# Kernel tuning notes

Measured on AMD Instinct MI355X. Metric: run time of the kernel, lower is better.

Reference implementation:

```python
import jax, jax.numpy as jnp
import numpy as np

B, P, J, MOT, K, NB, WN, H = 64, 12273, 80, 94, 64, 20, 17, 128
W_POSE = 1.0

def euler_to_rotmat(a):
    # a: [..., 3] radians, R = Rz @ Ry @ Rx
    sx, sy, sz = jnp.sin(a[..., 0]), jnp.sin(a[..., 1]), jnp.sin(a[..., 2])
    cx, cy, cz = jnp.cos(a[..., 0]), jnp.cos(a[..., 1]), jnp.cos(a[..., 2])
    r00 = cz * cy; r01 = cz * sy * sx - sz * cx; r02 = cz * sy * cx + sz * sx
    r10 = sz * cy; r11 = sz * sy * sx + cz * cx; r12 = sz * sy * cx - cz * sx
    r20 = -sy;     r21 = cy * sx;                r22 = cy * cx
    return jnp.stack([jnp.stack([r00, r01, r02], -1),
                      jnp.stack([r10, r11, r12], -1),
                      jnp.stack([r20, r21, r22], -1)], -2)

def setup_inputs() -> dict:
    key = jax.random.key(0)
    ks = jax.random.split(key, 20)
    f32 = jnp.float32
    return {
        'in_pc_batch': jax.random.normal(ks[0], (B, P, 3), f32),
        't_nor': jax.random.normal(ks[1], (B, P, 3), f32),
        'rest_verts': jax.random.normal(ks[2], (P, 3), f32),
        'skin_weights': jax.random.uniform(ks[3], (P, J), f32),
        'mul_weight_list': jax.random.normal(ks[4], (J, MOT), f32),
        'query': jax.random.normal(ks[5], (B, J, 3), f32),
        'cloth_pose_std': jax.random.uniform(ks[6], (3,), f32),
        'cloth_pose_mean': jax.random.normal(ks[7], (3,), f32),
        'cloth_trans_std': jax.random.uniform(ks[8], (3,), f32),
        'cloth_trans_mean': jax.random.normal(ks[9], (3,), f32),
        'W1': jax.random.normal(ks[10], (3 + K, H), f32) * 0.1,
        'b1': jnp.zeros((H,), f32),
        'W2': jax.random.normal(ks[11], (H, 6), f32) * 0.1,
        'b2': jnp.zeros((6,), f32),
        'tmtemp': jax.random.normal(ks[12], (B, MOT, K), f32),
        'Wd': jax.random.normal(ks[13], (MOT * K, NB * WN), f32) * 0.02,
        'bd': jnp.zeros((NB * WN,), f32),
        'DPSD': jax.random.normal(ks[14], (NB, WN, P, 3), f32) * 0.1,
        'ssdr_res_std': jax.random.uniform(ks[15], (3,), f32),
        'ssdr_res_mean': jax.random.normal(ks[16], (3,), f32),
    }

def reference(in_pc_batch, t_nor, rest_verts, skin_weights, mul_weight_list,
              query, cloth_pose_std, cloth_pose_mean, cloth_trans_std,
              cloth_trans_mean, W1, b1, W2, b2, tmtemp, Wd, bd, DPSD,
              ssdr_res_std, ssdr_res_mean):
    # per-joint field input: [B, J, K]
    field_input = jnp.einsum('bjk,lj->blk', tmtemp, jax.nn.relu(mul_weight_list))
    # FieldNet: per-joint MLP on concat(query, field_input) -> [B, J, 6]
    h = jnp.concatenate([query, field_input], axis=-1)
    pred_rt = jax.nn.relu(h @ W1 + b1) @ W2 + b2
    pred_pose = pred_rt[..., 0:3] * cloth_pose_std + cloth_pose_mean
    pred_trans = (query + pred_rt[..., 3:6]) * cloth_trans_std + cloth_trans_mean
    # detailsnet + fused 20-basis accumulation: [B, P, 3]
    nbat = tmtemp.shape[0]
    detailkey = (tmtemp.reshape(nbat, -1) @ Wd + bd).reshape(nbat, NB, WN)
    detail_res = jnp.einsum('bnw,nwpx->bpx', detailkey, DPSD)
    detail_res = detail_res * ssdr_res_std + ssdr_res_mean
    # SSDR LBS skinning with Euler-angle rotations (degrees -> radians)
    R = euler_to_rotmat(jnp.deg2rad(pred_pose))            # [B, J, 3, 3]
    skinned = (jnp.einsum('pj,bjxy,py->bpx', skin_weights, R, rest_verts)
               + jnp.einsum('pj,bjx->bpx', skin_weights, pred_trans))
    out_pc = skinned + detail_res                          # [B, P, 3]
    loss_pose_l1 = jnp.mean(jnp.abs(in_pc_batch[:, :, 0:3] - out_pc))
    loss = loss_pose_l1 * W_POSE + 1e-4 * jnp.mean(DPSD ** 2)
    return loss[None], out_pc
```

## Files before the change

kernel.cpp:

```cpp
#include <hip/hip_runtime.h>

#define B_   64
#define P_   12273
#define J_   80
#define MOT_ 94
#define K_   64
#define H_   128
#define Q_   340
#define NE_  36819
#define MK_  6016
#define PW_  12288

typedef float v4f  __attribute__((ext_vector_type(4)));
typedef float v8f  __attribute__((ext_vector_type(8)));
typedef float v16f __attribute__((ext_vector_type(16)));
#define AS4 __attribute__((address_space(4)))

__device__ __forceinline__ const AS4 float* unif(const float* p){
  return (const AS4 float*)(unsigned long long)p;
}
__device__ __forceinline__ const AS4 v4f* univ4(const float* p){
  return (const AS4 v4f*)(unsigned long long)p;
}
__device__ __forceinline__ const AS4 v8f* univ8(const float* p){
  return (const AS4 v8f*)(unsigned long long)p;
}
__device__ __forceinline__ const AS4 v16f* univ16(const float* p){
  return (const AS4 v16f*)(unsigned long long)p;
}

__global__ __launch_bounds__(256) void k_prep(
    const float* __restrict__ query, const float* __restrict__ mwl,
    const float* __restrict__ tm,    const float* __restrict__ W1,
    const float* __restrict__ b1,    const float* __restrict__ W2,
    const float* __restrict__ b2,    const float* __restrict__ cps,
    const float* __restrict__ cpm,   const float* __restrict__ cts,
    const float* __restrict__ ctm,   const float* __restrict__ skin,
    float* __restrict__ G,           float* __restrict__ tm_t,
    float* __restrict__ w_t,         float* __restrict__ lacc)
{
  __shared__ float smem[80 * 65];
  int blk = blockIdx.x;
  int t = threadIdx.x;
  if (blk < 1280){
    int lane = t & 63;
    int wid = __builtin_amdgcn_readfirstlane(t >> 6);
    int bj = blk * 4 + wid;
    int b = bj / J_, l = bj - b * J_;
    float* hs = smem + wid * 80;
    float acc = 0.f;
    const AS4 float* mp = unif(mwl + l * MOT_);
    const float* tp = tm + (size_t)b * MK_ + lane;
    #pragma unroll 2
    for (int j = 0; j < MOT_; j++){
      float w = mp[j]; w = w > 0.f ? w : 0.f;
      acc = fmaf(w, tp[j * K_], acc);
    }
    hs[3 + lane] = acc;
    if (lane < 3) hs[lane] = query[(size_t)bj * 3 + lane];
    __syncthreads();
    float a1 = b1[lane], a2 = b1[lane + 64];
    for (int i = 0; i < 3 + K_; i++){
      float hv = hs[i];
      a1 = fmaf(hv, W1[i * H_ + lane], a1);
      a2 = fmaf(hv, W1[i * H_ + 64 + lane], a2);
    }
    a1 = a1 > 0.f ? a1 : 0.f;
    a2 = a2 > 0.f ? a2 : 0.f;
    const AS4 float* b2c = unif(b2);
    float rt[6];
    #pragma unroll
    for (int o = 0; o < 6; o++){
      float po = fmaf(a1, W2[lane * 6 + o], a2 * W2[(lane + 64) * 6 + o]);
      #pragma unroll
      for (int off = 32; off; off >>= 1) po += __shfl_xor(po, off);
      rt[o] = po + b2c[o];
    }
    const float D2R = 0.017453292519943295f;
    float ax = fmaf(rt[0], cps[0], cpm[0]) * D2R;
    float ay = fmaf(rt[1], cps[1], cpm[1]) * D2R;
    float az = fmaf(rt[2], cps[2], cpm[2]) * D2R;
    float tx = fmaf(hs[0] + rt[3], cts[0], ctm[0]);
    float ty = fmaf(hs[1] + rt[4], cts[1], ctm[1]);
    float tz = fmaf(hs[2] + rt[5], cts[2], ctm[2]);
    float sx, cx, sy, cy, sz, cz;
    sincosf(ax, &sx, &cx); sincosf(ay, &sy, &cy); sincosf(az, &sz, &cz);
    if (lane == 0){
      float4 r0 = make_float4(cz*cy, cz*sy*sx - sz*cx, cz*sy*cx + sz*sx, tx);
      float4 r1 = make_float4(sz*cy, sz*sy*sx + cz*cx, sz*sy*cx - cz*sx, ty);
      float4 r2 = make_float4(-sy,   cy*sx,            cy*cx,            tz);
      float4* g = (float4*)(G + (size_t)bj * 12);
      g[0] = r0; g[1] = r1; g[2] = r2;
    }
  } else if (blk < 1374){
    int m0 = (blk - 1280) * 64;
    int ml = t & 63, g = t >> 6;
    #pragma unroll
    for (int r = 0; r < 16; r++){
      int b = g * 16 + r;
      smem[ml * 65 + b] = tm[(size_t)b * MK_ + m0 + ml];
    }
    __syncthreads();
    int bl = t & 63;
    #pragma unroll
    for (int r = 0; r < 16; r++){
      int m = g * 16 + r;
      tm_t[(size_t)(m0 + m) * 64 + bl] = smem[m * 65 + bl];
    }
  } else if (blk < 1566){
    int p0 = (blk - 1374) * 64;
    #pragma unroll
    for (int k = 0; k < 20; k++){
      int idx = k * 256 + t;
      int pl = idx / 80, j = idx - pl * 80;
      int p = p0 + pl;
      smem[j * 65 + pl] = (p < P_) ? skin[(size_t)p * J_ + j] : 0.f;
    }
    __syncthreads();
    #pragma unroll
    for (int k = 0; k < 20; k++){
      int idx = k * 256 + t;
      int j = idx >> 6, pl = idx & 63;
      w_t[(size_t)j * PW_ + p0 + pl] = smem[j * 65 + pl];
    }
  } else {
    if (t < 2) lacc[t] = 0.f;
  }
}

__global__ __launch_bounds__(256) void k_dkey(
    const float* __restrict__ tm_t, const float* __restrict__ Wd,
    float* __restrict__ part)
{
  int t = threadIdx.x;
  int lane = t & 63;
  int wid = __builtin_amdgcn_readfirstlane(t >> 6);
  int qt = blockIdx.x;
  int q = qt * 64 + lane;
  bool vq = q < Q_;
  int m0 = blockIdx.y * 64;
  const AS4 v16f* tr = univ16(tm_t);
  float acc[16];
  #pragma unroll
  for (int i = 0; i < 16; i++) acc[i] = 0.f;
  float wbuf[4];
  #pragma unroll
  for (int i = 0; i < 4; i++)
    wbuf[i] = vq ? Wd[(size_t)(m0 + i) * Q_ + q] : 0.f;
  v16f tb0 = tr[(size_t)(m0 + 0) * 4 + wid];
  v16f tb1 = tr[(size_t)(m0 + 1) * 4 + wid];
  #pragma unroll 4
  for (int mm = 0; mm < 60; mm++){
    float wd = wbuf[mm & 3];
    wbuf[mm & 3] = vq ? Wd[(size_t)(m0 + mm + 4) * Q_ + q] : 0.f;
    v16f tv = tb0; tb0 = tb1;
    tb1 = tr[(size_t)(m0 + mm + 2) * 4 + wid];
    #pragma unroll
    for (int i = 0; i < 16; i++) acc[i] = fmaf(tv[i], wd, acc[i]);
  }
  #pragma unroll
  for (int mm = 60; mm < 64; mm++){
    float wd = wbuf[mm & 3];
    v16f tv = tb0; tb0 = tb1;
    if (mm < 62) tb1 = tr[(size_t)(m0 + mm + 2) * 4 + wid];
    #pragma unroll
    for (int i = 0; i < 16; i++) acc[i] = fmaf(tv[i], wd, acc[i]);
  }
  float* pb = part + ((size_t)blockIdx.y * 6 + qt) * 4096 + (size_t)(wid * 16) * 64;
  #pragma unroll
  for (int i = 0; i < 16; i++) pb[i * 64 + lane] = acc[i];
}

__global__ __launch_bounds__(256) void k_dkred(
    const float* __restrict__ part, const float* __restrict__ bd,
    float* __restrict__ dk_t, int S)
{
  int t = threadIdx.x;
  int jj = blockIdx.x * 32 + (t >> 3);
  int dl = t & 7;
  int b = jj / Q_, q = jj - b * Q_;
  int qt = q >> 6, ql = q & 63;
  const float* pp = part + (size_t)qt * 4096 + b * 64 + ql;
  float s = 0.f;
  for (int d = dl; d < S; d += 8) s += pp[(size_t)d * 6 * 4096];
  s += __shfl_xor(s, 1); s += __shfl_xor(s, 2); s += __shfl_xor(s, 4);
  if (dl == 0) dk_t[q * 64 + b] = bd[q] + s;
}

__global__ __launch_bounds__(512) void k_detail(
    const float* __restrict__ DPSD, const float* __restrict__ dk_t,
    float* __restrict__ stg0, float* __restrict__ out,
    float* __restrict__ lacc, int qn)
{
  int t = threadIdx.x;
  int lane = t & 63;
  int wid = __builtin_amdgcn_readfirstlane(t >> 6);
  int b0 = wid * 8;
  int e = blockIdx.x * 64 + lane;
  bool ve = e < NE_;
  int q0 = blockIdx.y * qn;
  const AS4 v8f* dkv = univ8(dk_t + b0);
  const float* Dp = DPSD + e;
  float acc[8];
  #pragma unroll
  for (int i = 0; i < 8; i++) acc[i] = 0.f;
  float sq = 0.f;
  float dc[5], dn[5];
  #pragma unroll
  for (int i = 0; i < 5; i++)
    dc[i] = ve ? Dp[(size_t)(q0 + i) * NE_] : 0.f;
  int ng = qn / 5;
  for (int g = 0; g < ng; g++){
    int qq = q0 + g * 5;
    if (g + 1 < ng){
      #pragma unroll
      for (int i = 0; i < 5; i++)
        dn[i] = ve ? Dp[(size_t)(qq + 5 + i) * NE_] : 0.f;
    }
    v8f r0 = dkv[(qq + 0) * 8];
    v8f r1 = dkv[(qq + 1) * 8];
    v8f r2 = dkv[(qq + 2) * 8];
    v8f r3 = dkv[(qq + 3) * 8];
    v8f r4 = dkv[(qq + 4) * 8];
    if (wid == 0){
      #pragma unroll
      for (int i = 0; i < 5; i++) sq = fmaf(dc[i], dc[i], sq);
    }
    #pragma unroll
    for (int i = 0; i < 8; i++){
      acc[i] = fmaf(r0[i], dc[0], acc[i]);
      acc[i] = fmaf(r1[i], dc[1], acc[i]);
      acc[i] = fmaf(r2[i], dc[2], acc[i]);
      acc[i] = fmaf(r3[i], dc[3], acc[i]);
      acc[i] = fmaf(r4[i], dc[4], acc[i]);
    }
    #pragma unroll
    for (int i = 0; i < 5; i++) dc[i] = dn[i];
  }
  if (ve){
    bool toOut = (blockIdx.y + 1 == gridDim.y);
    float* dst = toOut ? (out + 1 + e) : (stg0 + e);
    #pragma unroll
    for (int i = 0; i < 8; i++)
      dst[(size_t)(b0 + i) * NE_] = acc[i];
  }
  if (wid == 0){
    #pragma unroll
    for (int off = 32; off; off >>= 1) sq += __shfl_xor(sq, off);
    if (lane == 0) atomicAdd(&lacc[1], sq);
  }
}

__global__ __launch_bounds__(256) void k_skin(
    const float* __restrict__ G, const float* __restrict__ w_t,
    const float* __restrict__ rest, const float* __restrict__ in_pc,
    const float* __restrict__ stg0, const float* __restrict__ rstd,
    const float* __restrict__ rmean,
    float* __restrict__ out, float* __restrict__ lacc, int two)
{
  int t = threadIdx.x;
  int lane = t & 63;
  int wid = __builtin_amdgcn_readfirstlane(t >> 6);
  int p  = blockIdx.x * 64 + lane;
  int bA = blockIdx.y * 8 + wid * 2;
  const AS4 v4f* gA = univ4(G + (size_t)bA * J_ * 12);
  const AS4 v4f* gB = univ4(G + ((size_t)bA + 1) * J_ * 12);
  float accA[12], accB[12];
  #pragma unroll
  for (int c = 0; c < 12; c++){ accA[c] = 0.f; accB[c] = 0.f; }
  const float* wp = w_t + p;
  #pragma unroll 4
  for (int j = 0; j < J_; j++){
    float w = wp[(size_t)j * PW_];
    v4f a0 = gA[j * 3 + 0], a1 = gA[j * 3 + 1], a2 = gA[j * 3 + 2];
    v4f c0 = gB[j * 3 + 0], c1 = gB[j * 3 + 1], c2 = gB[j * 3 + 2];
    #pragma unroll
    for (int c = 0; c < 4; c++){
      accA[c]     = fmaf(w, a0[c], accA[c]);
      accA[4 + c] = fmaf(w, a1[c], accA[4 + c]);
      accA[8 + c] = fmaf(w, a2[c], accA[8 + c]);
      accB[c]     = fmaf(w, c0[c], accB[c]);
      accB[4 + c] = fmaf(w, c1[c], accB[4 + c]);
      accB[8 + c] = fmaf(w, c2[c], accB[8 + c]);
    }
  }
  bool vp = p < P_;
  float vx = 0.f, vy = 0.f, vz = 0.f;
  if (vp){ vx = rest[p * 3]; vy = rest[p * 3 + 1]; vz = rest[p * 3 + 2]; }
  float srs[3], srm[3];
  #pragma unroll
  for (int x = 0; x < 3; x++){ srs[x] = rstd[x]; srm[x] = rmean[x]; }
  float lsum = 0.f;
  if (vp){
    size_t baseA = ((size_t)bA * P_ + p) * 3;
    size_t baseB = baseA + (size_t)P_ * 3;
    #pragma unroll
    for (int x = 0; x < 3; x++){
      float det = out[1 + baseA + x];
      if (two) det += stg0[baseA + x];
      float v = fmaf(accA[x*4+0], vx, fmaf(accA[x*4+1], vy, fmaf(accA[x*4+2], vz, accA[x*4+3])));
      v += fmaf(det, srs[x], srm[x]);
      lsum += fabsf(in_pc[baseA + x] - v);
      out[1 + baseA + x] = v;
    }
    #pragma unroll
    for (int x = 0; x < 3; x++){
      float det = out[1 + baseB + x];
      if (two) det += stg0[baseB + x];
      float v = fmaf(accB[x*4+0], vx, fmaf(accB[x*4+1], vy, fmaf(accB[x*4+2], vz, accB[x*4+3])));
      v += fmaf(det, srs[x], srm[x]);
      lsum += fabsf(in_pc[baseB + x] - v);
      out[1 + baseB + x] = v;
    }
  }
  #pragma unroll
  for (int off = 32; off; off >>= 1) lsum += __shfl_xor(lsum, off);
  __shared__ float red[4];
  if (lane == 0) red[wid] = lsum;
  __syncthreads();
  if (t == 0) atomicAdd(&lacc[0], red[0] + red[1] + red[2] + red[3]);
}

__global__ void k_finalize(const float* __restrict__ lacc, float* __restrict__ out){
  if (threadIdx.x == 0 && blockIdx.x == 0){
    float loss = lacc[0] * (1.f / 2356416.f) + 1e-4f * (lacc[1] * (1.f / 12518460.f));
    out[0] = loss;
  }
}

extern "C" void kernel_launch(void* const* d_in, const int* in_sizes, int n_in,
                              void* d_out, int out_size, void* d_ws, size_t ws_size,
                              hipStream_t stream){
  const float* in_pc = (const float*)d_in[0];
  const float* rest  = (const float*)d_in[2];
  const float* skin  = (const float*)d_in[3];
  const float* mwl   = (const float*)d_in[4];
  const float* query = (const float*)d_in[5];
  const float* cps   = (const float*)d_in[6];
  const float* cpm   = (const float*)d_in[7];
  const float* cts   = (const float*)d_in[8];
  const float* ctm   = (const float*)d_in[9];
  const float* W1    = (const float*)d_in[10];
  const float* b1    = (const float*)d_in[11];
  const float* W2    = (const float*)d_in[12];
  const float* b2    = (const float*)d_in[13];
  const float* tm    = (const float*)d_in[14];
  const float* Wd    = (const float*)d_in[15];
  const float* bd    = (const float*)d_in[16];
  const float* DPSD  = (const float*)d_in[17];
  const float* rstd  = (const float*)d_in[18];
  const float* rmean = (const float*)d_in[19];
  float* out = (float*)d_out;

  float* ws   = (float*)d_ws;
  float* G    = ws;
  float* dk_t = G + 61440;
  float* lacc = dk_t + 21760;
  float* tm_t = lacc + 64;
  float* w_t  = tm_t + 385024;
  float* un   = w_t + 983040;

  size_t have = ws_size / 4;
  int nqh = (have >= (size_t)(1451328 + 2356416)) ? 2 : 1;
  int qn = Q_ / nqh;

  k_prep    <<<1567, 256, 0, stream>>>(query, mwl, tm, W1, b1, W2, b2,
                                       cps, cpm, cts, ctm, skin,
                                       G, tm_t, w_t, lacc);
  k_dkey    <<<dim3(6, 94), 256, 0, stream>>>(tm_t, Wd, un);
  k_dkred   <<<680, 256, 0, stream>>>(un, bd, dk_t, 94);
  k_detail  <<<dim3(576, nqh), 512, 0, stream>>>(DPSD, dk_t, un, out, lacc, qn);
  k_skin    <<<dim3(192, 8), 256, 0, stream>>>(G, w_t, rest, in_pc, un, rstd, rmean,
                                               out, lacc, nqh - 1);
  k_finalize<<<1, 64, 0, stream>>>(lacc, out);
}
```

Baseline: 268.4 us.

## Stage detail keys in LDS and compute two element columns per thread

The detail kernel now copies its half of the detail-key table into shared memory once per block and reads it from LDS, where it previously used scalar/uniform global vector loads. Each thread now handles two DPSD columns (e and e+64), so every key value loaded is reused twice and the grid shrinks to 288x2 blocks. The split into two q halves is hardcoded, so the fallback that checked workspace size for a single-pass path is gone. The trade-offs are lower occupancy from the larger per-thread accumulators and LDS use, and reliance on the workspace always being large enough.

Measured after the change: 270.4 us. About the same (+0.7%).

```diff
diff --git a/kernel.cpp b/kernel.cpp
--- a/kernel.cpp
+++ b/kernel.cpp
@@ -10,6 +10,7 @@
 #define NE_  36819
 #define MK_  6016
 #define PW_  12288
+#define QH_  170
 
 typedef float v4f  __attribute__((ext_vector_type(4)));
 typedef float v8f  __attribute__((ext_vector_type(8)));
@@ -21,9 +22,6 @@
 }
 __device__ __forceinline__ const AS4 v4f* univ4(const float* p){
   return (const AS4 v4f*)(unsigned long long)p;
-}
-__device__ __forceinline__ const AS4 v8f* univ8(const float* p){
-  return (const AS4 v8f*)(unsigned long long)p;
 }
 __device__ __forceinline__ const AS4 v16f* univ16(const float* p){
   return (const AS4 v16f*)(unsigned long long)p;
@@ -190,59 +188,80 @@
 __global__ __launch_bounds__(512) void k_detail(
     const float* __restrict__ DPSD, const float* __restrict__ dk_t,
     float* __restrict__ stg0, float* __restrict__ out,
-    float* __restrict__ lacc, int qn)
-{
+    float* __restrict__ lacc)
+{
+  __shared__ float lds[QH_ * 64];
   int t = threadIdx.x;
   int lane = t & 63;
   int wid = __builtin_amdgcn_readfirstlane(t >> 6);
   int b0 = wid * 8;
-  int e = blockIdx.x * 64 + lane;
-  bool ve = e < NE_;
-  int q0 = blockIdx.y * qn;
-  const AS4 v8f* dkv = univ8(dk_t + b0);
+  int e  = blockIdx.x * 128 + lane;
+  int e2 = e + 64;
+  bool v2 = e2 < NE_;
+  int q0 = blockIdx.y * QH_;
+  {
+    const float4* src = (const float4*)(dk_t + (size_t)q0 * 64);
+    float4* dst = (float4*)lds;
+    for (int i = t; i < QH_ * 16; i += 512) dst[i] = src[i];
+  }
+  __syncthreads();
   const float* Dp = DPSD + e;
-  float acc[8];
-  #pragma unroll
-  for (int i = 0; i < 8; i++) acc[i] = 0.f;
+  float acc[8][2];
+  #pragma unroll
+  for (int i = 0; i < 8; i++){ acc[i][0] = 0.f; acc[i][1] = 0.f; }
   float sq = 0.f;
-  float dc[5], dn[5];
-  #pragma unroll
-  for (int i = 0; i < 5; i++)
-    dc[i] = ve ? Dp[(size_t)(q0 + i) * NE_] : 0.f;
-  int ng = qn / 5;
-  for (int g = 0; g < ng; g++){
-    int qq = q0 + g * 5;
-    if (g + 1 < ng){
+  float dcA[5], dcB[5], dnA[5], dnB[5];
+  #pragma unroll
+  for (int i = 0; i < 5; i++){
+    size_t ro = (size_t)(q0 + i) * NE_;
+    dcA[i] = Dp[ro];
+    dcB[i] = v2 ? Dp[ro + 64] : 0.f;
+  }
+  const int NG = QH_ / 5;
+  for (int g = 0; g < NG; g++){
+    int qq = g * 5;
+    if (g + 1 < NG){
       #pragma unroll
-      for (int i = 0; i < 5; i++)
-        dn[i] = ve ? Dp[(size_t)(qq + 5 + i) * NE_] : 0.f;
-    }
-    v8f r0 = dkv[(qq + 0) * 8];
-    v8f r1 = dkv[(qq + 1) * 8];
-    v8f r2 = dkv[(qq + 2) * 8];
-    v8f r3 = dkv[(qq + 3) * 8];
-    v8f r4 = dkv[(qq + 4) * 8];
+      for (int i = 0; i < 5; i++){
+        size_t ro = (size_t)(q0 + qq + 5 + i) * NE_;
+        dnA[i] = Dp[ro];
+        dnB[i] = v2 ? Dp[ro + 64] : 0.f;
+      }
+    }
     if (wid == 0){
       #pragma unroll
-      for (int i = 0; i < 5; i++) sq = fmaf(dc[i], dc[i], sq);
-    }
+      for (int i = 0; i < 5; i++){
+        sq = fmaf(dcA[i], dcA[i], sq);
+        sq = fmaf(dcB[i], dcB[i], sq);
+      }
+    }
+    #pragma unroll
+    for (int i = 0; i < 5; i++){
+      const float4* lp = (const float4*)(lds + (qq + i) * 64 + b0);
+      float4 r0 = lp[0];
+      float4 r1 = lp[1];
+      float dA = dcA[i], dB = dcB[i];
+      acc[0][0] = fmaf(r0.x, dA, acc[0][0]); acc[0][1] = fmaf(r0.x, dB, acc[0][1]);
+      acc[1][0] = fmaf(r0.y, dA, acc[1][0]); acc[1][1] = fmaf(r0.y, dB, acc[1][1]);
+      acc[2][0] = fmaf(r0.z, dA, acc[2][0]); acc[2][1] = fmaf(r0.z, dB, acc[2][1]);
+      acc[3][0] = fmaf(r0.w, dA, acc[3][0]); acc[3][1] = fmaf(r0.w, dB, acc[3][1]);
+      acc[4][0] = fmaf(r1.x, dA, acc[4][0]); acc[4][1] = fmaf(r1.x, dB, acc[4][1]);
+      acc[5][0] = fmaf(r1.y, dA, acc[5][0]); acc[5][1] = fmaf(r1.y, dB, acc[5][1]);
+      acc[6][0] = fmaf(r1.z, dA, acc[6][0]); acc[6][1] = fmaf(r1.z, dB, acc[6][1]);
+      acc[7][0] = fmaf(r1.w, dA, acc[7][0]); acc[7][1] = fmaf(r1.w, dB, acc[7][1]);
+    }
+    #pragma unroll
+    for (int i = 0; i < 5; i++){ dcA[i] = dnA[i]; dcB[i] = dnB[i]; }
+  }
+  {
+    bool toOut = (blockIdx.y == 1);
+    float* dst = toOut ? (out + 1) : stg0;
     #pragma unroll
     for (int i = 0; i < 8; i++){
-      acc[i] = fmaf(r0[i], dc[0], acc[i]);
-      acc[i] = fmaf(r1[i], dc[1], acc[i]);
-      acc[i] = fmaf(r2[i], dc[2], acc[i]);
-      acc[i] = fmaf(r3[i], dc[3], acc[i]);
-      acc[i] = fmaf(r4[i], dc[4], acc[i]);
-    }
-    #pragma unroll
-    for (int i = 0; i < 5; i++) dc[i] = dn[i];
-  }
-  if (ve){
-    bool toOut = (blockIdx.y + 1 == gridDim.y);
-    float* dst = toOut ? (out + 1 + e) : (stg0 + e);
-    #pragma unroll
-    for (int i = 0; i < 8; i++)
-      dst[(size_t)(b0 + i) * NE_] = acc[i];
+      size_t rb = (size_t)(b0 + i) * NE_;
+      dst[rb + e] = acc[i][0];
+      if (v2) dst[rb + e2] = acc[i][1];
+    }
   }
   if (wid == 0){
     #pragma unroll
@@ -256,7 +275,7 @@
     const float* __restrict__ rest, const float* __restrict__ in_pc,
     const float* __restrict__ stg0, const float* __restrict__ rstd,
     const float* __restrict__ rmean,
-    float* __restrict__ out, float* __restrict__ lacc, int two)
+    float* __restrict__ out, float* __restrict__ lacc)
 {
   int t = threadIdx.x;
   int lane = t & 63;
@@ -296,8 +315,7 @@
     size_t baseB = baseA + (size_t)P_ * 3;
     #pragma unroll
     for (int x = 0; x < 3; x++){
-      float det = out[1 + baseA + x];
-      if (two) det += stg0[baseA + x];
+      float det = out[1 + baseA + x] + stg0[baseA + x];
       float v = fmaf(accA[x*4+0], vx, fmaf(accA[x*4+1], vy, fmaf(accA[x*4+2], vz, accA[x*4+3])));
       v += fmaf(det, srs[x], srm[x]);
       lsum += fabsf(in_pc[baseA + x] - v);
@@ -305,8 +323,7 @@
     }
     #pragma unroll
     for (int x = 0; x < 3; x++){
-      float det = out[1 + baseB + x];
-      if (two) det += stg0[baseB + x];
+      float det = out[1 + baseB + x] + stg0[baseB + x];
       float v = fmaf(accB[x*4+0], vx, fmaf(accB[x*4+1], vy, fmaf(accB[x*4+2], vz, accB[x*4+3])));
       v += fmaf(det, srs[x], srm[x]);
       lsum += fabsf(in_pc[baseB + x] - v);
@@ -360,17 +377,13 @@
   float* w_t  = tm_t + 385024;
   float* un   = w_t + 983040;
 
-  size_t have = ws_size / 4;
-  int nqh = (have >= (size_t)(1451328 + 2356416)) ? 2 : 1;
-  int qn = Q_ / nqh;
-
   k_prep    <<<1567, 256, 0, stream>>>(query, mwl, tm, W1, b1, W2, b2,
                                        cps, cpm, cts, ctm, skin,
                                        G, tm_t, w_t, lacc);
   k_dkey    <<<dim3(6, 94), 256, 0, stream>>>(tm_t, Wd, un);
   k_dkred   <<<680, 256, 0, stream>>>(un, bd, dk_t, 94);
-  k_detail  <<<dim3(576, nqh), 512, 0, stream>>>(DPSD, dk_t, un, out, lacc, qn);
+  k_detail  <<<dim3(288, 2), 512, 0, stream>>>(DPSD, dk_t, un, out, lacc);
   k_skin    <<<dim3(192, 8), 256, 0, stream>>>(G, w_t, rest, in_pc, un, rstd, rmean,
-                                               out, lacc, nqh - 1);
+                                               out, lacc);
   k_finalize<<<1, 64, 0, stream>>>(lacc, out);
 }
```
